# Performance work log

Hardware: AMD Instinct MI355X
Metric: run time of the kernel (lower is better)

The kernel has to match this reference:

```python
import jax, jax.numpy as jnp
import numpy as np

H = 768      # hidden size
F = 3072     # FFN intermediate (4*H)
E = 8        # num experts
K = 2        # top_k
B, S = 2, 2048


def setup_inputs() -> dict:
    key = jax.random.key(0)
    ks = jax.random.split(key, 6)
    scale_in = 1.0 / np.sqrt(H)
    scale_mid = 1.0 / np.sqrt(F)
    return {
        "x": jax.random.normal(ks[0], (B, S, H), dtype=jnp.float32),
        "gate_w": jax.random.normal(ks[1], (H, E), dtype=jnp.float32) * scale_in,
        "W1": jax.random.normal(ks[2], (E, H, F), dtype=jnp.float32) * scale_in,
        "b1": jnp.zeros((E, F), dtype=jnp.float32),
        "W2": jax.random.normal(ks[3], (E, F, H), dtype=jnp.float32) * scale_mid,
        "b2": jnp.zeros((E, H), dtype=jnp.float32),
    }


def reference(x, gate_w, W1, b1, W2, b2):
    """MoE FFN: top-k router -> per-expert FFN -> weighted combine.

    Faithful to the torch module: router logits = x @ gate_w (no bias),
    softmax over the top-k logits only, each expert is a dense FFN
    (Linear -> GELU -> Linear), output = sum_k w_k * expert_{idx_k}(x).
    Expressed densely: combine weights are scattered into a [T, E] matrix
    (zero for unselected experts), so running every expert on every token
    and contracting with the combine matrix yields identical math.
    """
    batch, seq_len, hidden = x.shape
    xf = x.reshape(-1, hidden)                       # [T, H]
    T = xf.shape[0]

    logits = xf @ gate_w                             # [T, E]
    top_w, top_idx = jax.lax.top_k(logits, K)        # [T, K]
    top_w = jax.nn.softmax(top_w, axis=-1)

    # scatter top-k softmax weights into dense [T, E] combine matrix
    comb = jnp.zeros((T, E), dtype=x.dtype).at[
        jnp.arange(T)[:, None], top_idx
    ].add(top_w)

    # all experts on all tokens (zero combine weight kills unselected)
    h = jnp.einsum('th,ehf->etf', xf, W1) + b1[:, None, :]   # [E, T, F]
    h = jax.nn.gelu(h)
    y = jnp.einsum('etf,efh->eth', h, W2) + b2[:, None, :]   # [E, T, H]

    out = jnp.einsum('te,eth->th', comb, y)                  # [T, H]
    return out.reshape(batch, seq_len, hidden)
```

## Files before the change

kernel.cpp:

```cpp
#include <hip/hip_runtime.h>

#define H 768
#define F 3072
#define NE 8
#define T 4096
#define NA 8192
#define TP 9216
#define NRB 72
#define BM 128
#define BK 64

typedef unsigned short ushort_t;
typedef __attribute__((ext_vector_type(8))) short bfx8;
typedef __attribute__((ext_vector_type(4))) float fx4;

__device__ __forceinline__ ushort_t f2bf(float f) {
    union { float f; unsigned u; } v; v.f = f;
    unsigned u = v.u;
    unsigned r = (u + 0x7fffu + ((u >> 16) & 1u)) >> 16;
    return (ushort_t)r;
}

__device__ __forceinline__ float gelu_tanh(float x) {
    const float c = 0.7978845608028654f;
    float z = c * (x + 0.044715f * x * x * x);
    float t = 1.0f - 2.0f / (__expf(2.0f * z) + 1.0f);
    return 0.5f * x * (1.0f + t);
}

__device__ __forceinline__ void g2l16(const void* g, void* l) {
    __builtin_amdgcn_global_load_lds(
        (__attribute__((address_space(1))) void*)g,
        (__attribute__((address_space(3))) void*)l, 16, 0, 0);
}

__global__ void router_k(const float* __restrict__ x, const float* __restrict__ gw,
                         int* __restrict__ tidx, float* __restrict__ twgt) {
    int t = blockIdx.x * 4 + (threadIdx.x >> 6);
    int lane = threadIdx.x & 63;
    const float* xr = x + (size_t)t * H;
    float acc[NE];
#pragma unroll
    for (int e = 0; e < NE; ++e) acc[e] = 0.f;
    for (int h = lane; h < H; h += 64) {
        float xv = xr[h];
        const float* g = gw + h * NE;
#pragma unroll
        for (int e = 0; e < NE; ++e) acc[e] += xv * g[e];
    }
#pragma unroll
    for (int off = 32; off > 0; off >>= 1) {
#pragma unroll
        for (int e = 0; e < NE; ++e) acc[e] += __shfl_down(acc[e], off);
    }
    if (lane == 0) {
        float l0 = -1e30f, l1 = -1e30f; int i0 = 0, i1 = 0;
#pragma unroll
        for (int e = 0; e < NE; ++e) {
            float v = acc[e];
            if (v > l0) { l1 = l0; i1 = i0; l0 = v; i0 = e; }
            else if (v > l1) { l1 = v; i1 = e; }
        }
        float w0 = 1.f / (1.f + __expf(l1 - l0));
        tidx[t * 2] = i0; tidx[t * 2 + 1] = i1;
        twgt[t * 2] = w0; twgt[t * 2 + 1] = 1.f - w0;
    }
}

__global__ void init_k(int* counts, int* tos) {
    int i = blockIdx.x * 256 + threadIdx.x;
    if (i < NE) counts[i] = 0;
    if (i < TP) tos[i] = -1;
}

__global__ void count_k(const int* __restrict__ tidx, int* counts) {
    int i = blockIdx.x * 256 + threadIdx.x;
    if (i < NA) atomicAdd(&counts[tidx[i]], 1);
}

__global__ void offsets_k(const int* __restrict__ counts, int* cursor,
                          int* rbe, int* rbs) {
    int off = 0, rb = 0;
    for (int e = 0; e < NE; ++e) {
        cursor[e] = off;
        int nrb = (counts[e] + BM - 1) / BM;
        for (int j = 0; j < nrb; ++j) { rbe[rb] = e; rbs[rb] = off + j * BM; ++rb; }
        off += nrb * BM;
    }
    for (; rb < 96; ++rb) rbe[rb] = -1;
}

__global__ void scatter_k(const int* __restrict__ tidx, int* cursor,
                          int* __restrict__ tos, int* __restrict__ aslot) {
    int i = blockIdx.x * 256 + threadIdx.x;
    if (i < NA) {
        int e = tidx[i];
        int slot = atomicAdd(&cursor[e], 1);
        tos[slot] = i >> 1;
        aslot[i] = slot;
    }
}

__global__ void gather_k(const float* __restrict__ x, const int* __restrict__ tos,
                         ushort_t* __restrict__ xg) {
    int i = blockIdx.x * 256 + threadIdx.x;
    int slot = i / (H / 8);
    int j = i % (H / 8);
    int tok = tos[slot];
    ushort_t v[8];
    if (tok < 0) {
#pragma unroll
        for (int q = 0; q < 8; ++q) v[q] = 0;
    } else {
        const float* src = x + (size_t)tok * H + j * 8;
#pragma unroll
        for (int q = 0; q < 8; ++q) v[q] = f2bf(src[q]);
    }
    *(bfx8*)&xg[(size_t)slot * H + j * 8] = *(const bfx8*)v;
}

__global__ void transpose_cast_k(const float* __restrict__ src, ushort_t* __restrict__ dst,
                                 int R, int C) {
    int e = blockIdx.z;
    src += (size_t)e * R * C;
    dst += (size_t)e * R * C;
    int c0 = blockIdx.x * 64, r0 = blockIdx.y * 64;
    __shared__ float tile[64][65];
    int tid = threadIdx.x;
    int cc = tid & 63, rr = tid >> 6;
#pragma unroll
    for (int rep = 0; rep < 16; ++rep) {
        int r = rep * 4 + rr;
        tile[r][cc] = src[(size_t)(r0 + r) * C + c0 + cc];
    }
    __syncthreads();
#pragma unroll
    for (int rep = 0; rep < 16; ++rep) {
        int c = rep * 4 + rr;
        dst[(size_t)(c0 + c) * R + r0 + cc] = f2bf(tile[cc][c]);
    }
}

template <int DO_GELU>
__global__ __launch_bounds__(256)
void gemm_k(const ushort_t* __restrict__ A, const ushort_t* __restrict__ Bt,
            const float* __restrict__ bias, void* __restrict__ Cout,
            const int* __restrict__ rbe, const int* __restrict__ rbs,
            int K, int N) {
    int rb = blockIdx.x;
    int e = rbe[rb];
    if (e < 0) return;
    int slot0 = rbs[rb];
    int n0 = blockIdx.y * 128;

    __shared__ __align__(16) ushort_t Al[BM * BK];
    __shared__ __align__(16) ushort_t Bl[BM * BK];

    int tid = threadIdx.x;
    int wid = tid >> 6, lane = tid & 63;
    int wr = wid >> 1, wc = wid & 1;

    fx4 zero = {0.f, 0.f, 0.f, 0.f};
    fx4 acc[4][4];
#pragma unroll
    for (int m = 0; m < 4; ++m)
#pragma unroll
        for (int n = 0; n < 4; ++n) acc[m][n] = zero;

    const ushort_t* Ab = A + (size_t)slot0 * K;
    const ushort_t* Bb = Bt + ((size_t)e * N + n0) * K;
    int rA = lane >> 3;
    int cA = (lane & 7) * 8;
    int l15 = lane & 15;
    int kh = (lane >> 4) * 8;

    for (int k0 = 0; k0 < K; k0 += BK) {
#pragma unroll
        for (int r = 0; r < 4; ++r) {
            int seg = r * 4 + wid;
            int row = seg * 8 + rA;
            g2l16(Ab + (size_t)row * K + k0 + cA, &Al[seg * 512]);
            g2l16(Bb + (size_t)row * K + k0 + cA, &Bl[seg * 512]);
        }
        __syncthreads();
#pragma unroll
        for (int kk = 0; kk < 2; ++kk) {
            bfx8 af[4], bv[4];
            int ko = kk * 32 + kh;
#pragma unroll
            for (int m = 0; m < 4; ++m)
                af[m] = *(const bfx8*)&Al[(wr * 64 + m * 16 + l15) * BK + ko];
#pragma unroll
            for (int n = 0; n < 4; ++n)
                bv[n] = *(const bfx8*)&Bl[(wc * 64 + n * 16 + l15) * BK + ko];
#pragma unroll
            for (int m = 0; m < 4; ++m)
#pragma unroll
                for (int n = 0; n < 4; ++n)
                    acc[m][n] = __builtin_amdgcn_mfma_f32_16x16x32_bf16(af[m], bv[n], acc[m][n], 0, 0, 0);
        }
        __syncthreads();
    }

    int col0 = n0 + wc * 64;
    int row0 = slot0 + wr * 64 + (lane >> 4) * 4;
#pragma unroll
    for (int n = 0; n < 4; ++n) {
        int col = col0 + n * 16 + l15;
        float bvv = bias[(size_t)e * N + col];
#pragma unroll
        for (int m = 0; m < 4; ++m) {
            int row = row0 + m * 16;
#pragma unroll
            for (int j = 0; j < 4; ++j) {
                float v = acc[m][n][j] + bvv;
                if (DO_GELU) {
                    ((ushort_t*)Cout)[(size_t)(row + j) * N + col] = f2bf(gelu_tanh(v));
                } else {
                    ((float*)Cout)[(size_t)(row + j) * N + col] = v;
                }
            }
        }
    }
}

__global__ void combine_k(const float* __restrict__ y, const int* __restrict__ aslot,
                          const float* __restrict__ twgt, float* __restrict__ out) {
    int i = blockIdx.x * 256 + threadIdx.x;
    int t = i / (H / 4);
    int j = i % (H / 4);
    int s0 = aslot[t * 2], s1 = aslot[t * 2 + 1];
    float w0 = twgt[t * 2], w1 = twgt[t * 2 + 1];
    const float4 a = ((const float4*)(y + (size_t)s0 * H))[j];
    const float4 b = ((const float4*)(y + (size_t)s1 * H))[j];
    float4 r;
    r.x = w0 * a.x + w1 * b.x;
    r.y = w0 * a.y + w1 * b.y;
    r.z = w0 * a.z + w1 * b.z;
    r.w = w0 * a.w + w1 * b.w;
    ((float4*)(out + (size_t)t * H))[j] = r;
}

extern "C" void kernel_launch(void* const* d_in, const int* in_sizes, int n_in,
                              void* d_out, int out_size, void* d_ws, size_t ws_size,
                              hipStream_t stream) {
    const float* x  = (const float*)d_in[0];
    const float* gw = (const float*)d_in[1];
    const float* W1 = (const float*)d_in[2];
    const float* b1 = (const float*)d_in[3];
    const float* W2 = (const float*)d_in[4];
    const float* b2 = (const float*)d_in[5];
    float* out = (float*)d_out;

    char* ws = (char*)d_ws;
    size_t o = 0;
    auto carve = [&](size_t bytes) -> void* {
        o = (o + 255) & ~(size_t)255;
        void* p = ws + o;
        o += bytes;
        return p;
    };
    int*      tidx   = (int*)carve((size_t)NA * 4);
    float*    twgt   = (float*)carve((size_t)NA * 4);
    int*      counts = (int*)carve(NE * 4);
    int*      cursor = (int*)carve(NE * 4);
    int*      rbe    = (int*)carve(96 * 4);
    int*      rbs    = (int*)carve(96 * 4);
    int*      aslot  = (int*)carve((size_t)NA * 4);
    int*      tos    = (int*)carve((size_t)TP * 4);
    ushort_t* xg     = (ushort_t*)carve((size_t)TP * H * 2);
    ushort_t* w1t    = (ushort_t*)carve((size_t)NE * H * F * 2);
    ushort_t* w2t    = (ushort_t*)carve((size_t)NE * H * F * 2);
    ushort_t* hbuf   = (ushort_t*)carve((size_t)TP * F * 2);
    float*    ybuf   = (float*)carve((size_t)TP * H * 4);
    (void)in_sizes; (void)n_in; (void)out_size; (void)ws_size;

    hipLaunchKernelGGL(init_k, dim3(TP / 256), dim3(256), 0, stream, counts, tos);
    hipLaunchKernelGGL(router_k, dim3(T / 4), dim3(256), 0, stream, x, gw, tidx, twgt);
    hipLaunchKernelGGL(count_k, dim3(NA / 256), dim3(256), 0, stream, tidx, counts);
    hipLaunchKernelGGL(offsets_k, dim3(1), dim3(1), 0, stream, counts, cursor, rbe, rbs);
    hipLaunchKernelGGL(scatter_k, dim3(NA / 256), dim3(256), 0, stream, tidx, cursor, tos, aslot);
    hipLaunchKernelGGL(gather_k, dim3(TP * (H / 8) / 256), dim3(256), 0, stream, x, tos, xg);
    hipLaunchKernelGGL(transpose_cast_k, dim3(F / 64, H / 64, NE), dim3(256), 0, stream, W1, w1t, H, F);
    hipLaunchKernelGGL(transpose_cast_k, dim3(H / 64, F / 64, NE), dim3(256), 0, stream, W2, w2t, F, H);
    hipLaunchKernelGGL((gemm_k<1>), dim3(NRB, F / 128), dim3(256), 0, stream,
                       xg, w1t, b1, (void*)hbuf, rbe, rbs, H, F);
    hipLaunchKernelGGL((gemm_k<0>), dim3(NRB, H / 128), dim3(256), 0, stream,
                       hbuf, w2t, b2, (void*)ybuf, rbe, rbs, F, H);
    hipLaunchKernelGGL(combine_k, dim3(T * (H / 4) / 256), dim3(256), 0, stream,
                       ybuf, aslot, twgt, out);
}
```

Baseline: 308.0 us.

## Replace grouped GEMM with 256x256 double-buffered, swizzled, ping-pong scheduled kernel

Replaces the 128x128 single-buffered grouped expert GEMM with a 256x256-tile, 512-thread kernel. It double-buffers LDS tiles fetched by direct global-to-LDS loads, XOR-swizzles LDS columns, and interleaves staging with MFMA quads using explicit waitcnt, barriers and priority hints. It also remaps workgroup IDs across XCDs and pads expert row blocks to 256. The intent is to cut LDS traffic per flop and hide memory latency. In exchange, padding waste rises to at most 40 row blocks, and the y buffer now aliases the gathered-input buffer to save workspace.

```diff
diff --git a/kernel.cpp b/kernel.cpp
--- a/kernel.cpp
+++ b/kernel.cpp
@@ -5,10 +5,8 @@
 #define NE 8
 #define T 4096
 #define NA 8192
-#define TP 9216
-#define NRB 72
-#define BM 128
-#define BK 64
+#define TP 10240
+#define NRB 40
 
 typedef unsigned short ushort_t;
 typedef __attribute__((ext_vector_type(8))) short bfx8;
@@ -33,6 +31,13 @@
         (__attribute__((address_space(1))) void*)g,
         (__attribute__((address_space(3))) void*)l, 16, 0, 0);
 }
+
+#define WAITV(N) asm volatile("s_waitcnt vmcnt(" #N ")" ::: "memory")
+#define LGKM0    asm volatile("s_waitcnt lgkmcnt(0)" ::: "memory")
+#define SBAR     __builtin_amdgcn_s_barrier()
+#define SCHED0   __builtin_amdgcn_sched_barrier(0)
+#define PRIO1    __builtin_amdgcn_s_setprio(1)
+#define PRIO0    __builtin_amdgcn_s_setprio(0)
 
 __global__ void router_k(const float* __restrict__ x, const float* __restrict__ gw,
                          int* __restrict__ tidx, float* __restrict__ twgt) {
@@ -83,11 +88,11 @@
     int off = 0, rb = 0;
     for (int e = 0; e < NE; ++e) {
         cursor[e] = off;
-        int nrb = (counts[e] + BM - 1) / BM;
-        for (int j = 0; j < nrb; ++j) { rbe[rb] = e; rbs[rb] = off + j * BM; ++rb; }
-        off += nrb * BM;
-    }
-    for (; rb < 96; ++rb) rbe[rb] = -1;
+        int nrb = (counts[e] + 255) / 256;
+        for (int j = 0; j < nrb; ++j) { rbe[rb] = e; rbs[rb] = off + j * 256; ++rb; }
+        off += nrb * 256;
+    }
+    for (; rb < NRB; ++rb) rbe[rb] = -1;
 }
 
 __global__ void scatter_k(const int* __restrict__ tidx, int* cursor,
@@ -142,86 +147,158 @@
 }
 
 template <int DO_GELU>
-__global__ __launch_bounds__(256)
-void gemm_k(const ushort_t* __restrict__ A, const ushort_t* __restrict__ Bt,
-            const float* __restrict__ bias, void* __restrict__ Cout,
-            const int* __restrict__ rbe, const int* __restrict__ rbs,
-            int K, int N) {
-    int rb = blockIdx.x;
+__global__ __launch_bounds__(512, 2)
+void gemm256_k(const ushort_t* __restrict__ A, const ushort_t* __restrict__ Bt,
+               const float* __restrict__ bias, void* __restrict__ Cout,
+               const int* __restrict__ rbe, const int* __restrict__ rbs,
+               int K, int N, int ncb) {
+    int nwg = gridDim.x;
+    int bid = blockIdx.x;
+    int wgid = (bid & 7) * (nwg >> 3) + (bid >> 3);
+    int rb = wgid / ncb, cb = wgid % ncb;
     int e = rbe[rb];
     if (e < 0) return;
     int slot0 = rbs[rb];
-    int n0 = blockIdx.y * 128;
-
-    __shared__ __align__(16) ushort_t Al[BM * BK];
-    __shared__ __align__(16) ushort_t Bl[BM * BK];
+
+    __shared__ __align__(16) ushort_t lds[65536];
 
     int tid = threadIdx.x;
-    int wid = tid >> 6, lane = tid & 63;
-    int wr = wid >> 1, wc = wid & 1;
-
-    fx4 zero = {0.f, 0.f, 0.f, 0.f};
-    fx4 acc[4][4];
-#pragma unroll
-    for (int m = 0; m < 4; ++m)
-#pragma unroll
-        for (int n = 0; n < 4; ++n) acc[m][n] = zero;
+    int lane = tid & 63, wid = tid >> 6;
+    int wr = wid >> 2, wc = wid & 3;
+    int l15 = lane & 15, qh = lane >> 4, sw = l15 & 7;
 
     const ushort_t* Ab = A + (size_t)slot0 * K;
-    const ushort_t* Bb = Bt + ((size_t)e * N + n0) * K;
-    int rA = lane >> 3;
-    int cA = (lane & 7) * 8;
-    int l15 = lane & 15;
-    int kh = (lane >> 4) * 8;
-
-    for (int k0 = 0; k0 < K; k0 += BK) {
-#pragma unroll
-        for (int r = 0; r < 4; ++r) {
-            int seg = r * 4 + wid;
-            int row = seg * 8 + rA;
-            g2l16(Ab + (size_t)row * K + k0 + cA, &Al[seg * 512]);
-            g2l16(Bb + (size_t)row * K + k0 + cA, &Bl[seg * 512]);
-        }
-        __syncthreads();
-#pragma unroll
-        for (int kk = 0; kk < 2; ++kk) {
-            bfx8 af[4], bv[4];
-            int ko = kk * 32 + kh;
-#pragma unroll
-            for (int m = 0; m < 4; ++m)
-                af[m] = *(const bfx8*)&Al[(wr * 64 + m * 16 + l15) * BK + ko];
-#pragma unroll
-            for (int n = 0; n < 4; ++n)
-                bv[n] = *(const bfx8*)&Bl[(wc * 64 + n * 16 + l15) * BK + ko];
-#pragma unroll
-            for (int m = 0; m < 4; ++m)
-#pragma unroll
-                for (int n = 0; n < 4; ++n)
-                    acc[m][n] = __builtin_amdgcn_mfma_f32_16x16x32_bf16(af[m], bv[n], acc[m][n], 0, 0, 0);
-        }
-        __syncthreads();
-    }
-
-    int col0 = n0 + wc * 64;
-    int row0 = slot0 + wr * 64 + (lane >> 4) * 4;
-#pragma unroll
-    for (int n = 0; n < 4; ++n) {
-        int col = col0 + n * 16 + l15;
-        float bvv = bias[(size_t)e * N + col];
-#pragma unroll
-        for (int m = 0; m < 4; ++m) {
-            int row = row0 + m * 16;
-#pragma unroll
-            for (int j = 0; j < 4; ++j) {
-                float v = acc[m][n][j] + bvv;
-                if (DO_GELU) {
-                    ((ushort_t*)Cout)[(size_t)(row + j) * N + col] = f2bf(gelu_tanh(v));
-                } else {
-                    ((float*)Cout)[(size_t)(row + j) * N + col] = v;
+    const ushort_t* Bb = Bt + ((size_t)e * N + cb * 256) * K;
+
+    int ar = (wr * 64 + l15) * 64;
+    int br = 16384 + (wc * 32 + l15) * 64;
+    int ch[2]; ch[0] = ((0 * 4 + qh) ^ sw) << 3; ch[1] = ((1 * 4 + qh) ^ sw) << 3;
+
+    unsigned offA0r0, offA0r1, offB0r0, offB0r1;
+    {
+        int idx0 = tid, idx1 = 512 + tid;
+        int j0 = idx0 >> 3, q0 = idx0 & 7, cs0 = q0 ^ (j0 & 7);
+        int j1 = idx1 >> 3, q1 = idx1 & 7, cs1 = q1 ^ (j1 & 7);
+        offA0r0 = (unsigned)((((j0 >> 6) << 7) + (j0 & 63)) * K + cs0 * 8);
+        offA0r1 = (unsigned)((((j1 >> 6) << 7) + (j1 & 63)) * K + cs1 * 8);
+        offB0r0 = (unsigned)((((j0 >> 5) << 6) + (j0 & 31)) * K + cs0 * 8);
+        offB0r1 = (unsigned)((((j1 >> 5) << 6) + (j1 & 31)) * K + cs1 * 8);
+    }
+    unsigned dA = (unsigned)(64 * K), dB = (unsigned)(32 * K);
+    int ldsw = wid * 512;
+
+#define STAGE_A(BUF, HH, KT) do { \
+    g2l16(Ab + (size_t)(offA0r0 + (HH) * dA + (unsigned)((KT) * 64)), &lds[(BUF) * 32768 + (HH) * 8192 + ldsw]); \
+    g2l16(Ab + (size_t)(offA0r1 + (HH) * dA + (unsigned)((KT) * 64)), &lds[(BUF) * 32768 + (HH) * 8192 + 4096 + ldsw]); \
+} while (0)
+#define STAGE_B(BUF, HH, KT) do { \
+    g2l16(Bb + (size_t)(offB0r0 + (HH) * dB + (unsigned)((KT) * 64)), &lds[(BUF) * 32768 + 16384 + (HH) * 8192 + ldsw]); \
+    g2l16(Bb + (size_t)(offB0r1 + (HH) * dB + (unsigned)((KT) * 64)), &lds[(BUF) * 32768 + 16384 + (HH) * 8192 + 4096 + ldsw]); \
+} while (0)
+#define LDA(BUF, MH) do { \
+    _Pragma("unroll") for (int m = 0; m < 4; ++m) \
+    _Pragma("unroll") for (int kk = 0; kk < 2; ++kk) \
+        a[m * 2 + kk] = *(const bfx8*)&lds[(BUF) * 32768 + (MH) * 8192 + ar + m * 1024 + ch[kk]]; \
+} while (0)
+#define LDB(BUF, NH, ARR) do { \
+    _Pragma("unroll") for (int n = 0; n < 2; ++n) \
+    _Pragma("unroll") for (int kk = 0; kk < 2; ++kk) \
+        ARR[n * 2 + kk] = *(const bfx8*)&lds[(BUF) * 32768 + (NH) * 8192 + br + n * 1024 + ch[kk]]; \
+} while (0)
+#define QUAD(MH, NH, ARR) do { \
+    _Pragma("unroll") for (int kk = 0; kk < 2; ++kk) \
+    _Pragma("unroll") for (int m = 0; m < 4; ++m) \
+    _Pragma("unroll") for (int n = 0; n < 2; ++n) \
+        acc[(MH) * 4 + m][(NH) * 2 + n] = __builtin_amdgcn_mfma_f32_16x16x32_bf16( \
+            a[m * 2 + kk], ARR[n * 2 + kk], acc[(MH) * 4 + m][(NH) * 2 + n], 0, 0, 0); \
+} while (0)
+
+    fx4 acc[8][4];
+#pragma unroll
+    for (int m = 0; m < 8; ++m)
+#pragma unroll
+        for (int n = 0; n < 4; ++n) acc[m][n] = (fx4){0.f, 0.f, 0.f, 0.f};
+    bfx8 a[8], b0[4], b1[4];
+
+    STAGE_A(0, 0, 0); STAGE_A(0, 1, 0); STAGE_B(0, 0, 0); STAGE_B(0, 1, 0);
+    STAGE_B(1, 0, 1); STAGE_A(1, 0, 1); STAGE_B(1, 1, 1);
+    WAITV(6);
+    SBAR;
+
+    int nit = K >> 7;
+    for (int it = 0; it < nit; ++it) {
+        int k1 = 2 * it + 1, kt2 = 2 * it + 2, kt3 = 2 * it + 3;
+        bool notlast = (it + 1 < nit);
+        LDA(0, 0); LDB(0, 0, b0);
+        STAGE_A(1, 1, k1);
+        SBAR; LGKM0; SCHED0;
+        PRIO1; QUAD(0, 0, b0); PRIO0;
+        SBAR;
+        LDB(0, 1, b1);
+        if (notlast) STAGE_B(0, 0, kt2);
+        SBAR; LGKM0; SCHED0;
+        PRIO1; QUAD(0, 1, b1); PRIO0;
+        SBAR;
+        LDA(0, 1);
+        if (notlast) STAGE_A(0, 0, kt2);
+        SBAR; LGKM0; SCHED0;
+        PRIO1; QUAD(1, 1, b1); PRIO0;
+        SBAR;
+        if (notlast) { STAGE_B(0, 1, kt2); WAITV(6); }
+        else WAITV(0);
+        SBAR; SCHED0;
+        PRIO1; QUAD(1, 0, b0); PRIO0;
+        SBAR;
+        LDA(1, 0); LDB(1, 0, b0);
+        if (notlast) STAGE_A(0, 1, kt2);
+        SBAR; LGKM0; SCHED0;
+        PRIO1; QUAD(0, 0, b0); PRIO0;
+        SBAR;
+        LDB(1, 1, b1);
+        if (notlast) STAGE_B(1, 0, kt3);
+        SBAR; LGKM0; SCHED0;
+        PRIO1; QUAD(0, 1, b1); PRIO0;
+        SBAR;
+        LDA(1, 1);
+        if (notlast) STAGE_A(1, 0, kt3);
+        SBAR; LGKM0; SCHED0;
+        PRIO1; QUAD(1, 1, b1); PRIO0;
+        SBAR;
+        if (notlast) { STAGE_B(1, 1, kt3); WAITV(6); }
+        else WAITV(0);
+        SBAR; SCHED0;
+        PRIO1; QUAD(1, 0, b0); PRIO0;
+        SBAR;
+    }
+
+#pragma unroll
+    for (int mh = 0; mh < 2; ++mh)
+#pragma unroll
+        for (int nh = 0; nh < 2; ++nh)
+#pragma unroll
+            for (int n = 0; n < 2; ++n) {
+                int col = cb * 256 + wc * 64 + nh * 32 + n * 16 + l15;
+                float bvv = bias[(size_t)e * N + col];
+#pragma unroll
+                for (int m = 0; m < 4; ++m) {
+                    int rowb = slot0 + wr * 128 + mh * 64 + m * 16 + qh * 4;
+                    fx4 v = acc[mh * 4 + m][nh * 2 + n];
+#pragma unroll
+                    for (int j = 0; j < 4; ++j) {
+                        float val = v[j] + bvv;
+                        if (DO_GELU) {
+                            ((ushort_t*)Cout)[(size_t)(rowb + j) * N + col] = f2bf(gelu_tanh(val));
+                        } else {
+                            ((float*)Cout)[(size_t)(rowb + j) * N + col] = val;
+                        }
+                    }
                 }
             }
-        }
-    }
+#undef STAGE_A
+#undef STAGE_B
+#undef LDA
+#undef LDB
+#undef QUAD
 }
 
 __global__ void combine_k(const float* __restrict__ y, const int* __restrict__ aslot,
@@ -264,15 +341,15 @@
     float*    twgt   = (float*)carve((size_t)NA * 4);
     int*      counts = (int*)carve(NE * 4);
     int*      cursor = (int*)carve(NE * 4);
-    int*      rbe    = (int*)carve(96 * 4);
-    int*      rbs    = (int*)carve(96 * 4);
+    int*      rbe    = (int*)carve(NRB * 4);
+    int*      rbs    = (int*)carve(NRB * 4);
     int*      aslot  = (int*)carve((size_t)NA * 4);
     int*      tos    = (int*)carve((size_t)TP * 4);
     ushort_t* xg     = (ushort_t*)carve((size_t)TP * H * 2);
     ushort_t* w1t    = (ushort_t*)carve((size_t)NE * H * F * 2);
     ushort_t* w2t    = (ushort_t*)carve((size_t)NE * H * F * 2);
     ushort_t* hbuf   = (ushort_t*)carve((size_t)TP * F * 2);
-    float*    ybuf   = (float*)carve((size_t)TP * H * 4);
+    float*    ybuf   = (float*)xg;
     (void)in_sizes; (void)n_in; (void)out_size; (void)ws_size;
 
     hipLaunchKernelGGL(init_k, dim3(TP / 256), dim3(256), 0, stream, counts, tos);
@@ -283,10 +360,10 @@
     hipLaunchKernelGGL(gather_k, dim3(TP * (H / 8) / 256), dim3(256), 0, stream, x, tos, xg);
     hipLaunchKernelGGL(transpose_cast_k, dim3(F / 64, H / 64, NE), dim3(256), 0, stream, W1, w1t, H, F);
     hipLaunchKernelGGL(transpose_cast_k, dim3(H / 64, F / 64, NE), dim3(256), 0, stream, W2, w2t, F, H);
-    hipLaunchKernelGGL((gemm_k<1>), dim3(NRB, F / 128), dim3(256), 0, stream,
-                       xg, w1t, b1, (void*)hbuf, rbe, rbs, H, F);
-    hipLaunchKernelGGL((gemm_k<0>), dim3(NRB, H / 128), dim3(256), 0, stream,
-                       hbuf, w2t, b2, (void*)ybuf, rbe, rbs, F, H);
+    hipLaunchKernelGGL((gemm256_k<1>), dim3(NRB * (F / 256)), dim3(512), 0, stream,
+                       xg, w1t, b1, (void*)hbuf, rbe, rbs, H, F, F / 256);
+    hipLaunchKernelGGL((gemm256_k<0>), dim3(NRB * (H / 256)), dim3(512), 0, stream,
+                       hbuf, w2t, b2, (void*)ybuf, rbe, rbs, F, H, H / 256);
     hipLaunchKernelGGL(combine_k, dim3(T * (H / 4) / 256), dim3(256), 0, stream,
                        ybuf, aslot, twgt, out);
 }
```

Result: faster. 288.8 us (-6.2%).

## Rewrite expert GEMMs with triple-buffered LDS pipeline, swizzle and larger tiles

Applied to the files above, without the earlier changes.

Replaces the single-buffered 128x128 grouped GEMM with a 512-thread kernel that uses a three-stage global-to-LDS ring. It waits with explicit vmcnt/lgkmcnt, XOR-swizzles LDS to avoid bank conflicts, raises priority around the MFMA blocks and remaps workgroup IDs across XCDs. Tiles grow to 128x256 for the first GEMM and 256x128 for the second, with expert padding raised to 256 rows. The aim is to overlap loads with MFMA and reuse more data per tile. The cost is extra padded rows, hand-written waitcnt logic that may be fragile, and ybuf now aliasing the xg buffer.

```diff
diff --git a/kernel.cpp b/kernel.cpp
--- a/kernel.cpp
+++ b/kernel.cpp
@@ -5,14 +5,14 @@
 #define NE 8
 #define T 4096
 #define NA 8192
-#define TP 9216
-#define NRB 72
-#define BM 128
-#define BK 64
+#define TP 10240
+#define NRB2 40
+#define NRB1 80
 
 typedef unsigned short ushort_t;
 typedef __attribute__((ext_vector_type(8))) short bfx8;
 typedef __attribute__((ext_vector_type(4))) float fx4;
+typedef __attribute__((address_space(3))) const ushort_t lus;
 
 __device__ __forceinline__ ushort_t f2bf(float f) {
     union { float f; unsigned u; } v; v.f = f;
@@ -33,6 +33,21 @@
         (__attribute__((address_space(1))) void*)g,
         (__attribute__((address_space(3))) void*)l, 16, 0, 0);
 }
+
+__device__ __forceinline__ bfx8 dsr128(lus* p) {
+    bfx8 r;
+    asm volatile("ds_read_b128 %0, %1" : "=v"(r) : "v"(p));
+    return r;
+}
+
+#define WAITV6 asm volatile("s_waitcnt vmcnt(6)" ::: "memory")
+#define WAITV0 asm volatile("s_waitcnt vmcnt(0)" ::: "memory")
+#define LGKM8  asm volatile("s_waitcnt lgkmcnt(8)" ::: "memory")
+#define LGKM0  asm volatile("s_waitcnt lgkmcnt(0)" ::: "memory")
+#define SBAR   __builtin_amdgcn_s_barrier()
+#define SCHED0 __builtin_amdgcn_sched_barrier(0)
+#define PRIO1  __builtin_amdgcn_s_setprio(1)
+#define PRIO0  __builtin_amdgcn_s_setprio(0)
 
 __global__ void router_k(const float* __restrict__ x, const float* __restrict__ gw,
                          int* __restrict__ tidx, float* __restrict__ twgt) {
@@ -79,15 +94,20 @@
 }
 
 __global__ void offsets_k(const int* __restrict__ counts, int* cursor,
-                          int* rbe, int* rbs) {
-    int off = 0, rb = 0;
+                          int* rbe2, int* rbs2, int* rbe1, int* rbs1) {
+    int off = 0, rb2 = 0, rb1 = 0;
     for (int e = 0; e < NE; ++e) {
         cursor[e] = off;
-        int nrb = (counts[e] + BM - 1) / BM;
-        for (int j = 0; j < nrb; ++j) { rbe[rb] = e; rbs[rb] = off + j * BM; ++rb; }
-        off += nrb * BM;
-    }
-    for (; rb < 96; ++rb) rbe[rb] = -1;
+        int nrb = (counts[e] + 255) / 256;
+        for (int j = 0; j < nrb; ++j) {
+            rbe2[rb2] = e; rbs2[rb2] = off + j * 256; ++rb2;
+            rbe1[rb1] = e; rbs1[rb1] = off + j * 256; ++rb1;
+            rbe1[rb1] = e; rbs1[rb1] = off + j * 256 + 128; ++rb1;
+        }
+        off += nrb * 256;
+    }
+    for (; rb2 < NRB2; ++rb2) rbe2[rb2] = -1;
+    for (; rb1 < NRB1; ++rb1) rbe1[rb1] = -1;
 }
 
 __global__ void scatter_k(const int* __restrict__ tidx, int* cursor,
@@ -141,87 +161,113 @@
     }
 }
 
-template <int DO_GELU>
-__global__ __launch_bounds__(256)
-void gemm_k(const ushort_t* __restrict__ A, const ushort_t* __restrict__ Bt,
-            const float* __restrict__ bias, void* __restrict__ Cout,
-            const int* __restrict__ rbe, const int* __restrict__ rbs,
-            int K, int N) {
-    int rb = blockIdx.x;
+template <int WM, int WN, int DO_GELU>
+__global__ __launch_bounds__(512, 2)
+void gemm_tile_k(const ushort_t* __restrict__ A, const ushort_t* __restrict__ Bt,
+                 const float* __restrict__ bias, void* __restrict__ Cout,
+                 const int* __restrict__ rbe, const int* __restrict__ rbs,
+                 int K, int N, int ncb) {
+    constexpr int BM = WM * 64, BN = WN * 64;
+    constexpr int UA = BM / 64, UB = BN / 64;
+    constexpr int BUFS = (BM + BN) * 64;
+
+    int nwg = gridDim.x, bid = blockIdx.x;
+    int wgid = (bid & 7) * (nwg >> 3) + (bid >> 3);
+    int rb = wgid / ncb, cb = wgid % ncb;
     int e = rbe[rb];
     if (e < 0) return;
     int slot0 = rbs[rb];
-    int n0 = blockIdx.y * 128;
-
-    __shared__ __align__(16) ushort_t Al[BM * BK];
-    __shared__ __align__(16) ushort_t Bl[BM * BK];
-
-    int tid = threadIdx.x;
-    int wid = tid >> 6, lane = tid & 63;
-    int wr = wid >> 1, wc = wid & 1;
-
-    fx4 zero = {0.f, 0.f, 0.f, 0.f};
+
+    __shared__ __align__(16) ushort_t lds[3 * BUFS];
+
+    int tid = threadIdx.x, lane = tid & 63, wid = tid >> 6;
+    int wm = wid / WN, wn = wid % WN;
+    int l15 = lane & 15, qh = lane >> 4, sw = l15 & 7;
+
+    const ushort_t* Ab = A + (size_t)slot0 * K;
+    const ushort_t* Bb = Bt + ((size_t)e * N + cb * BN) * K;
+
+    int j = tid >> 3, q = tid & 7;
+    int cs = (q ^ (j & 7)) * 8;
+    int ldsw = wid * 512;
+
+    int ch0 = ((0 * 4 + qh) ^ sw) << 3;
+    int ch1 = ((1 * 4 + qh) ^ sw) << 3;
+    int abase = (wm * 64 + l15) * 64;
+    int bbase = BM * 64 + (wn * 64 + l15) * 64;
+
+#define STAGE_T(NB, KT) do { \
+    _Pragma("unroll") for (int u = 0; u < UA; ++u) \
+        g2l16(Ab + (size_t)(u * 64 + j) * K + (KT) * 64 + cs, \
+              &lds[(NB) * BUFS + u * 4096 + ldsw]); \
+    _Pragma("unroll") for (int u = 0; u < UB; ++u) \
+        g2l16(Bb + (size_t)(u * 64 + j) * K + (KT) * 64 + cs, \
+              &lds[(NB) * BUFS + BM * 64 + u * 4096 + ldsw]); \
+} while (0)
+
     fx4 acc[4][4];
 #pragma unroll
     for (int m = 0; m < 4; ++m)
 #pragma unroll
-        for (int n = 0; n < 4; ++n) acc[m][n] = zero;
-
-    const ushort_t* Ab = A + (size_t)slot0 * K;
-    const ushort_t* Bb = Bt + ((size_t)e * N + n0) * K;
-    int rA = lane >> 3;
-    int cA = (lane & 7) * 8;
-    int l15 = lane & 15;
-    int kh = (lane >> 4) * 8;
-
-    for (int k0 = 0; k0 < K; k0 += BK) {
-#pragma unroll
-        for (int r = 0; r < 4; ++r) {
-            int seg = r * 4 + wid;
-            int row = seg * 8 + rA;
-            g2l16(Ab + (size_t)row * K + k0 + cA, &Al[seg * 512]);
-            g2l16(Bb + (size_t)row * K + k0 + cA, &Bl[seg * 512]);
-        }
-        __syncthreads();
-#pragma unroll
-        for (int kk = 0; kk < 2; ++kk) {
-            bfx8 af[4], bv[4];
-            int ko = kk * 32 + kh;
-#pragma unroll
-            for (int m = 0; m < 4; ++m)
-                af[m] = *(const bfx8*)&Al[(wr * 64 + m * 16 + l15) * BK + ko];
+        for (int n = 0; n < 4; ++n) acc[m][n] = (fx4){0.f, 0.f, 0.f, 0.f};
+    bfx8 a0[4], a1[4], b0v[4], b1v[4];
+
+    int NT = K >> 6;
+    STAGE_T(0, 0);
+    STAGE_T(1, 1);
+
+    for (int t = 0; t < NT; ++t) {
+        int nb = t % 3;
+        if (t + 1 < NT) { WAITV6; } else { WAITV0; }
+        SBAR;
+        int ab = nb * BUFS + abase, bb = nb * BUFS + bbase;
+#pragma unroll
+        for (int m = 0; m < 4; ++m) a0[m] = dsr128((lus*)&lds[ab + m * 1024 + ch0]);
+#pragma unroll
+        for (int n = 0; n < 4; ++n) b0v[n] = dsr128((lus*)&lds[bb + n * 1024 + ch0]);
+#pragma unroll
+        for (int m = 0; m < 4; ++m) a1[m] = dsr128((lus*)&lds[ab + m * 1024 + ch1]);
+#pragma unroll
+        for (int n = 0; n < 4; ++n) b1v[n] = dsr128((lus*)&lds[bb + n * 1024 + ch1]);
+        if (t + 2 < NT) STAGE_T((t + 2) % 3, t + 2);
+        LGKM8; SCHED0;
+        PRIO1;
+#pragma unroll
+        for (int m = 0; m < 4; ++m)
 #pragma unroll
             for (int n = 0; n < 4; ++n)
-                bv[n] = *(const bfx8*)&Bl[(wc * 64 + n * 16 + l15) * BK + ko];
-#pragma unroll
-            for (int m = 0; m < 4; ++m)
-#pragma unroll
-                for (int n = 0; n < 4; ++n)
-                    acc[m][n] = __builtin_amdgcn_mfma_f32_16x16x32_bf16(af[m], bv[n], acc[m][n], 0, 0, 0);
-        }
-        __syncthreads();
-    }
-
-    int col0 = n0 + wc * 64;
-    int row0 = slot0 + wr * 64 + (lane >> 4) * 4;
+                acc[m][n] = __builtin_amdgcn_mfma_f32_16x16x32_bf16(a0[m], b0v[n], acc[m][n], 0, 0, 0);
+        PRIO0;
+        LGKM0; SCHED0;
+        PRIO1;
+#pragma unroll
+        for (int m = 0; m < 4; ++m)
+#pragma unroll
+            for (int n = 0; n < 4; ++n)
+                acc[m][n] = __builtin_amdgcn_mfma_f32_16x16x32_bf16(a1[m], b1v[n], acc[m][n], 0, 0, 0);
+        PRIO0;
+    }
+
 #pragma unroll
     for (int n = 0; n < 4; ++n) {
-        int col = col0 + n * 16 + l15;
+        int col = cb * BN + wn * 64 + n * 16 + l15;
         float bvv = bias[(size_t)e * N + col];
 #pragma unroll
         for (int m = 0; m < 4; ++m) {
-            int row = row0 + m * 16;
-#pragma unroll
-            for (int j = 0; j < 4; ++j) {
-                float v = acc[m][n][j] + bvv;
+            int rowb = slot0 + wm * 64 + m * 16 + qh * 4;
+            fx4 v = acc[m][n];
+#pragma unroll
+            for (int jj = 0; jj < 4; ++jj) {
+                float val = v[jj] + bvv;
                 if (DO_GELU) {
-                    ((ushort_t*)Cout)[(size_t)(row + j) * N + col] = f2bf(gelu_tanh(v));
+                    ((ushort_t*)Cout)[(size_t)(rowb + jj) * N + col] = f2bf(gelu_tanh(val));
                 } else {
-                    ((float*)Cout)[(size_t)(row + j) * N + col] = v;
+                    ((float*)Cout)[(size_t)(rowb + jj) * N + col] = val;
                 }
             }
         }
     }
+#undef STAGE_T
 }
 
 __global__ void combine_k(const float* __restrict__ y, const int* __restrict__ aslot,
@@ -264,29 +310,32 @@
     float*    twgt   = (float*)carve((size_t)NA * 4);
     int*      counts = (int*)carve(NE * 4);
     int*      cursor = (int*)carve(NE * 4);
-    int*      rbe    = (int*)carve(96 * 4);
-    int*      rbs    = (int*)carve(96 * 4);
+    int*      rbe2   = (int*)carve(NRB2 * 4);
+    int*      rbs2   = (int*)carve(NRB2 * 4);
+    int*      rbe1   = (int*)carve(NRB1 * 4);
+    int*      rbs1   = (int*)carve(NRB1 * 4);
     int*      aslot  = (int*)carve((size_t)NA * 4);
     int*      tos    = (int*)carve((size_t)TP * 4);
     ushort_t* xg     = (ushort_t*)carve((size_t)TP * H * 2);
     ushort_t* w1t    = (ushort_t*)carve((size_t)NE * H * F * 2);
     ushort_t* w2t    = (ushort_t*)carve((size_t)NE * H * F * 2);
     ushort_t* hbuf   = (ushort_t*)carve((size_t)TP * F * 2);
-    float*    ybuf   = (float*)carve((size_t)TP * H * 4);
+    float*    ybuf   = (float*)xg;
     (void)in_sizes; (void)n_in; (void)out_size; (void)ws_size;
 
     hipLaunchKernelGGL(init_k, dim3(TP / 256), dim3(256), 0, stream, counts, tos);
     hipLaunchKernelGGL(router_k, dim3(T / 4), dim3(256), 0, stream, x, gw, tidx, twgt);
     hipLaunchKernelGGL(count_k, dim3(NA / 256), dim3(256), 0, stream, tidx, counts);
-    hipLaunchKernelGGL(offsets_k, dim3(1), dim3(1), 0, stream, counts, cursor, rbe, rbs);
+    hipLaunchKernelGGL(offsets_k, dim3(1), dim3(1), 0, stream, counts, cursor,
+                       rbe2, rbs2, rbe1, rbs1);
     hipLaunchKernelGGL(scatter_k, dim3(NA / 256), dim3(256), 0, stream, tidx, cursor, tos, aslot);
     hipLaunchKernelGGL(gather_k, dim3(TP * (H / 8) / 256), dim3(256), 0, stream, x, tos, xg);
     hipLaunchKernelGGL(transpose_cast_k, dim3(F / 64, H / 64, NE), dim3(256), 0, stream, W1, w1t, H, F);
     hipLaunchKernelGGL(transpose_cast_k, dim3(H / 64, F / 64, NE), dim3(256), 0, stream, W2, w2t, F, H);
-    hipLaunchKernelGGL((gemm_k<1>), dim3(NRB, F / 128), dim3(256), 0, stream,
-                       xg, w1t, b1, (void*)hbuf, rbe, rbs, H, F);
-    hipLaunchKernelGGL((gemm_k<0>), dim3(NRB, H / 128), dim3(256), 0, stream,
-                       hbuf, w2t, b2, (void*)ybuf, rbe, rbs, F, H);
+    hipLaunchKernelGGL((gemm_tile_k<2, 4, 1>), dim3(NRB1 * (F / 256)), dim3(512), 0, stream,
+                       xg, w1t, b1, (void*)hbuf, rbe1, rbs1, H, F, F / 256);
+    hipLaunchKernelGGL((gemm_tile_k<4, 2, 0>), dim3(NRB2 * (H / 128)), dim3(512), 0, stream,
+                       hbuf, w2t, b2, (void*)ybuf, rbe2, rbs2, F, H, H / 128);
     hipLaunchKernelGGL(combine_k, dim3(T * (H / 4) / 256), dim3(256), 0, stream,
                        ybuf, aslot, twgt, out);
 }
```

Measured after the change: 270.0 us. 1.14x faster.
